# Optimization experiments

Hardware: AMD Instinct MI355X
Metric: run time of the kernel (lower is better)

## Reference

```python
import jax, jax.numpy as jnp
import numpy as np

NUM_HEADS = 16


def rotate_half(x):
    x1 = x[..., ::2]
    x2 = x[..., 1::2]
    return jnp.concatenate((-x2, x1), axis=-1)


def rope_sin_cos(seq_len, head_dim, dtype):
    inv_freq = 1.0 / (10000.0 ** (jnp.arange(0, head_dim, 2, dtype=jnp.float32) / head_dim))
    t = jnp.arange(seq_len, dtype=jnp.float32)
    freqs = jnp.einsum('i,j->ij', t, inv_freq)          # [S, D/2]
    emb = jnp.concatenate((freqs, freqs), axis=-1)      # [S, D]
    return jnp.sin(emb).astype(dtype), jnp.cos(emb).astype(dtype)


def setup_inputs() -> dict:
    key = jax.random.key(0)
    B, S, E = 2, 2048, 2048
    ks = jax.random.split(key, 5)
    scale = 1.0 / np.sqrt(E)
    return {
        'x': jax.random.normal(ks[0], (B, S, E), dtype=jnp.float32),
        'mask': jnp.ones((B, S), dtype=jnp.int32),
        'Wq': jax.random.normal(ks[1], (E, E), dtype=jnp.float32) * scale,
        'bq': jnp.zeros((E,), dtype=jnp.float32),
        'Wk': jax.random.normal(ks[2], (E, E), dtype=jnp.float32) * scale,
        'bk': jnp.zeros((E,), dtype=jnp.float32),
        'Wv': jax.random.normal(ks[3], (E, E), dtype=jnp.float32) * scale,
        'bv': jnp.zeros((E,), dtype=jnp.float32),
        'Wo': jax.random.normal(ks[4], (E, E), dtype=jnp.float32) * scale,
        'bo': jnp.zeros((E,), dtype=jnp.float32),
    }


def reference(x, mask, Wq, bq, Wk, bk, Wv, bv, Wo, bo):
    B, S, E = x.shape
    H = NUM_HEADS
    D = E // H
    q = (x @ Wq + bq).reshape(B, S, H, D).transpose(0, 2, 1, 3)  # [B,H,S,D]
    k = (x @ Wk + bk).reshape(B, S, H, D).transpose(0, 2, 1, 3)
    v = (x @ Wv + bv).reshape(B, S, H, D).transpose(0, 2, 1, 3)

    sin, cos = rope_sin_cos(S, D, q.dtype)  # [S,D]
    sin = sin[None, None]                    # [1,1,S,D]
    cos = cos[None, None]
    q = q * cos + rotate_half(q) * sin
    k = k * cos + rotate_half(k) * sin

    scores = jnp.einsum('bhqd,bhkd->bhqk', q, k) / jnp.sqrt(jnp.asarray(D, q.dtype))
    scores = jnp.where(mask[:, None, None, :] == 0, -jnp.inf, scores)
    probs = jax.nn.softmax(scores, axis=-1)
    attn = jnp.einsum('bhqk,bhkd->bhqd', probs, v)       # [B,H,S,D]
    attn = attn.transpose(0, 2, 1, 3).reshape(B, S, E)
    return attn @ Wo + bo
```

## Files before the change

kernel.cpp:

```cpp
#include <hip/hip_runtime.h>
#include <hip/hip_bf16.h>
#include <cmath>

typedef unsigned short u16;
typedef unsigned int   u32;

using v4f    = __attribute__((ext_vector_type(4)))  float;
using f32x16 = __attribute__((ext_vector_type(16))) float;
using s8v    = __attribute__((ext_vector_type(8)))  short;
using u32x2  = __attribute__((ext_vector_type(2)))  unsigned int;

union Frag { uint4 u; s8v s; };

__device__ __forceinline__ u16 f2bf(float f){
  u32 u = __float_as_uint(f);
  u32 r = u + 0x7fffu + ((u >> 16) & 1u);
  return (u16)(r >> 16);
}
__device__ __forceinline__ float bf2f(u16 h){ return __uint_as_float(((u32)h) << 16); }
__device__ __forceinline__ u32 pkbf(float a, float b){
  return (u32)f2bf(a) | ((u32)f2bf(b) << 16);
}

__device__ __forceinline__ void async16(const void* g, void* l){
  __builtin_amdgcn_global_load_lds((__attribute__((address_space(1))) void*)g,
                                   (__attribute__((address_space(3))) void*)l, 16, 0, 0);
}

__global__ __launch_bounds__(256) void cast_x_kernel(const float* __restrict__ x, u16* __restrict__ xb){
  size_t i = ((size_t)blockIdx.x * 256 + threadIdx.x) * 4;
  float4 v = *(const float4*)(x + i);
  uint2 o;
  o.x = (u32)f2bf(v.x) | ((u32)f2bf(v.y) << 16);
  o.y = (u32)f2bf(v.z) | ((u32)f2bf(v.w) << 16);
  *(uint2*)(xb + i) = o;
}

__global__ __launch_bounds__(256) void cast_transpose_kernel(
    const float* __restrict__ W0, const float* __restrict__ W1,
    const float* __restrict__ W2, const float* __restrict__ W3,
    u16* __restrict__ T0, u16* __restrict__ T1, u16* __restrict__ T2, u16* __restrict__ T3){
  __shared__ float tile[64][65];
  const float* W = (blockIdx.z==0)?W0:(blockIdx.z==1)?W1:(blockIdx.z==2)?W2:W3;
  u16*         T = (blockIdx.z==0)?T0:(blockIdx.z==1)?T1:(blockIdx.z==2)?T2:T3;
  const int k0 = blockIdx.y*64, n0 = blockIdx.x*64;
  const int t  = threadIdx.x;
  const int rr = t >> 4, c4 = (t & 15) * 4;
  #pragma unroll
  for (int i=0;i<4;i++){
    int k = rr + i*16;
    float4 v = *(const float4*)(W + (size_t)(k0+k)*2048 + n0 + c4);
    tile[k][c4+0]=v.x; tile[k][c4+1]=v.y; tile[k][c4+2]=v.z; tile[k][c4+3]=v.w;
  }
  __syncthreads();
  #pragma unroll
  for (int i=0;i<4;i++){
    int n = rr + i*16;
    uint2 o;
    o.x = (u32)f2bf(tile[c4+0][n]) | ((u32)f2bf(tile[c4+1][n])<<16);
    o.y = (u32)f2bf(tile[c4+2][n]) | ((u32)f2bf(tile[c4+3][n])<<16);
    *(uint2*)(T + (size_t)(n0+n)*2048 + k0 + c4) = o;
  }
}

template<int MODE>
__global__ __launch_bounds__(256) void gemm_kernel(const u16* __restrict__ A,
                                                   const u16* __restrict__ BT,
                                                   const float* __restrict__ bias,
                                                   void* __restrict__ Cout){
  constexpr int K = 2048;
  __shared__ u16 Asl[128*64];
  __shared__ u16 Bsl[128*64];
  const int tid  = threadIdx.x;
  const int w    = tid >> 6;
  const int lane = tid & 63;
  const int r    = lane & 15, q = lane >> 4;
  const int m0   = blockIdx.y * 128;
  const int n0   = blockIdx.x * 128;
  const int wm   = (w >> 1) * 64, wn = (w & 1) * 64;

  v4f acc[4][4];
  #pragma unroll
  for (int i=0;i<4;i++)
    #pragma unroll
    for (int j=0;j<4;j++) acc[i][j] = (v4f)0.f;

  const int srow = w*32 + (lane>>3);
  const int sblk = (lane&7) ^ ((lane>>3)&7);
  const u16* Ag = A  + (size_t)(m0+srow)*K + sblk*8;
  const u16* Bg = BT + (size_t)(n0+srow)*K + sblk*8;
  u16* Als = Asl + (w*32)*64;
  u16* Bls = Bsl + (w*32)*64;

  for (int kk = 0; kk < K; kk += 64) {
    #pragma unroll
    for (int i=0;i<4;i++){
      async16(Ag + (size_t)i*8*K + kk, Als + i*512);
      async16(Bg + (size_t)i*8*K + kk, Bls + i*512);
    }
    __syncthreads();
    #pragma unroll
    for (int ks=0; ks<2; ++ks) {
      s8v af[4], bfr[4];
      #pragma unroll
      for (int i=0;i<4;i++){
        int rho = wm + i*16 + r;
        int p = (ks*4 + q) ^ (r&7);
        Frag t; t.u = *(const uint4*)(Asl + rho*64 + p*8); af[i] = t.s;
      }
      #pragma unroll
      for (int j=0;j<4;j++){
        int rho = wn + j*16 + r;
        int p = (ks*4 + q) ^ (r&7);
        Frag t; t.u = *(const uint4*)(Bsl + rho*64 + p*8); bfr[j] = t.s;
      }
      #pragma unroll
      for (int i=0;i<4;i++)
        #pragma unroll
        for (int j=0;j<4;j++)
          acc[i][j] = __builtin_amdgcn_mfma_f32_16x16x32_bf16(af[i], bfr[j], acc[i][j], 0, 0, 0);
    }
    __syncthreads();
  }

  float bv[4];
  #pragma unroll
  for (int j=0;j<4;j++) bv[j] = bias[n0 + wn + j*16 + r];

  #pragma unroll
  for (int i=0;i<4;i++){
    #pragma unroll
    for (int j=0;j<4;j++){
      const int gn = n0 + wn + j*16 + r;
      #pragma unroll
      for (int rr2=0; rr2<4; ++rr2){
        const int gm = m0 + wm + i*16 + q*4 + rr2;
        float val = acc[i][j][rr2] + bv[j];
        if (MODE == 0) ((u16*)Cout)[(size_t)gm*2048 + gn] = f2bf(val);
        else           ((float*)Cout)[(size_t)gm*2048 + gn] = val;
      }
    }
  }
}

__global__ __launch_bounds__(256) void rope_kernel(u16* __restrict__ Q, u16* __restrict__ Kb){
  const int wrow = blockIdx.x*4 + (threadIdx.x >> 6);
  const int lane = threadIdx.x & 63;
  u16* P = (blockIdx.y == 0) ? Q : Kb;
  const int s = (wrow >> 4) & 2047;
  const size_t base = (size_t)wrow * 128;
  float invf = exp2f(-(float)lane * 0.20762050593045952f);
  float angle = (float)s * invf;
  float sn, cs;
  sincosf(angle, &sn, &cs);
  float x_j   = bf2f(P[base + lane]);
  float x_j64 = bf2f(P[base + 64 + lane]);
  float x_2j  = bf2f(P[base + 2*lane]);
  float x_2j1 = bf2f(P[base + 2*lane + 1]);
  float o0 = x_j  * cs - x_2j1 * sn;
  float o1 = x_j64 * cs + x_2j  * sn;
  P[base + lane]      = f2bf(o0);
  P[base + 64 + lane] = f2bf(o1);
}

__global__ __launch_bounds__(256) void transpose_v_kernel(const u16* __restrict__ V, u16* __restrict__ VT){
  __shared__ u16 t[64*72];
  const int s0 = blockIdx.x*64;
  const int d0 = blockIdx.y*64;
  const int bh = blockIdx.z;
  const int b = bh >> 4, h = bh & 15;
  const size_t obase = ((size_t)bh*128 + d0)*2048 + s0;
  const int tid = threadIdx.x;
  #pragma unroll
  for (int i=0;i<2;i++){
    int c = tid + i*256;
    int sl = c >> 3, dc = (c & 7) * 8;
    *(uint4*)(t + sl*72 + dc) =
      *(const uint4*)(V + ((size_t)(b*2048 + s0 + sl))*2048 + h*128 + d0 + dc);
  }
  __syncthreads();
  #pragma unroll
  for (int i=0;i<2;i++){
    int c = tid + i*256;
    int dl = c >> 3, sc4 = (c & 7) * 8;
    u16 tmp[8];
    #pragma unroll
    for (int j=0;j<8;j++) tmp[j] = t[(sc4+j)*72 + dl];
    *(uint4*)(VT + obase + (size_t)dl*2048 + sc4) = *(const uint4*)tmp;
  }
}

__global__ __launch_bounds__(256,2) void attn_kernel(const u16* __restrict__ Q,
                                                     const u16* __restrict__ K,
                                                     const u16* __restrict__ VT,
                                                     const int* __restrict__ mask,
                                                     u16* __restrict__ Out){
  constexpr int S = 2048;
  constexpr float SL2 = 0.08838834764831845f * 1.4426950408889634f;
  __shared__ u16 smem[16384];
  u16* Ks = smem;
  u16* Vs = smem + 8192;

  const int tid = threadIdx.x, w = tid >> 6, lane = tid & 63;
  const int qc = lane & 31;
  const int h  = lane >> 5;
  const int l7 = lane & 7;
  const int hh = blockIdx.y, b = blockIdx.z;
  const int q0 = blockIdx.x * 128;
  const size_t rowb = (size_t)b * 2048;
  const size_t bhD  = ((size_t)(b*16 + hh)) * 128;

  s8v qf[8];
  {
    const u16* qp = Q + (rowb + q0 + w*32 + qc)*2048 + hh*128 + h*8;
    #pragma unroll
    for (int t=0;t<8;t++){ Frag f; f.u = *(const uint4*)(qp + t*16); qf[t] = f.s; }
  }

  f32x16 accO[4];
  #pragma unroll
  for (int d=0; d<4; d++) accO[d] = (f32x16)0.f;
  float lsum = 0.f;

  const int sr4 = lane >> 4, sp16 = lane & 15;
  const int vr8 = lane >> 3, vp8 = lane & 7;

  for (int it=0; it<32; ++it){
    const int key0 = it*64;
    #pragma unroll
    for (int i=0;i<4;i++){
      int R = w*16 + i*4;
      int ob = sp16 ^ ((R&7) + sr4);
      async16(K + (rowb + key0 + R + sr4)*2048 + hh*128 + ob*8, Ks + R*128);
    }
    #pragma unroll
    for (int i=0;i<4;i++){
      int R = w*32 + i*8;
      int ob = vp8 ^ vr8;
      async16(VT + (bhD + R + vr8)*2048 + key0 + ob*8, Vs + R*64);
    }
    unsigned long long bm = __ballot(mask[b*S + key0 + lane] != 0);
    __syncthreads();

    #pragma unroll
    for (int nb=0; nb<2; ++nb){
      f32x16 sc = (f32x16)0.f;
      #pragma unroll
      for (int t=0;t<8;t++){
        Frag kf; kf.u = *(const uint4*)(Ks + (nb*32 + qc)*128 + (((2*t + h) ^ l7)*8));
        sc = __builtin_amdgcn_mfma_f32_32x32x16_bf16(kf.s, qf[t], sc, 0, 0, 0);
      }
      float p[16];
      #pragma unroll
      for (int m=0; m<16; ++m) p[m] = exp2f(sc[m] * SL2);
      if (bm != ~0ull){
        #pragma unroll
        for (int m=0; m<16; ++m){
          int bit = nb*32 + (m&3) + 8*(m>>2) + 4*h;
          if (!((bm >> bit) & 1ull)) p[m] = 0.f;
        }
      }
      #pragma unroll
      for (int m=0; m<16; ++m) lsum += p[m];

      #pragma unroll
      for (int g=0; g<2; ++g){
        u32 a0 = pkbf(p[8*g+0], p[8*g+1]);
        u32 a1 = pkbf(p[8*g+2], p[8*g+3]);
        u32 a2 = pkbf(p[8*g+4], p[8*g+5]);
        u32 a3 = pkbf(p[8*g+6], p[8*g+7]);
        u32x2 r0 = __builtin_amdgcn_permlane32_swap(a0, a2, false, false);
        u32x2 r1 = __builtin_amdgcn_permlane32_swap(a1, a3, false, false);
        Frag pf; pf.u = make_uint4(r0[0], r1[0], r0[1], r1[1]);
        const int T = nb*2 + g;
        #pragma unroll
        for (int d=0; d<4; ++d){
          Frag vf; vf.u = *(const uint4*)(Vs + (d*32 + qc)*64 + (((2*T + h) ^ l7)*8));
          accO[d] = __builtin_amdgcn_mfma_f32_32x32x16_bf16(vf.s, pf.s, accO[d], 0, 0, 0);
        }
      }
    }
    __syncthreads();
  }

  float sall = lsum + __shfl_xor(lsum, 32, 64);
  float invv = (sall > 0.f) ? 1.f/sall : 0.f;
  u16* orow = Out + (rowb + q0 + w*32 + qc)*2048 + hh*128;
  #pragma unroll
  for (int d=0; d<4; ++d){
    #pragma unroll
    for (int g2=0; g2<4; ++g2){
      union { u16 q4[4]; uint2 u; } o;
      #pragma unroll
      for (int j=0;j<4;j++) o.q4[j] = f2bf(accO[d][g2*4+j] * invv);
      *(uint2*)(orow + d*32 + g2*8 + 4*h) = o.u;
    }
  }
}

extern "C" void kernel_launch(void* const* d_in, const int* in_sizes, int n_in,
                              void* d_out, int out_size, void* d_ws, size_t ws_size,
                              hipStream_t stream) {
  (void)in_sizes; (void)n_in; (void)out_size; (void)ws_size;
  const float* x    = (const float*)d_in[0];
  const int*   mask = (const int*)d_in[1];
  const float* Wq   = (const float*)d_in[2];
  const float* bq   = (const float*)d_in[3];
  const float* Wk   = (const float*)d_in[4];
  const float* bk   = (const float*)d_in[5];
  const float* Wv   = (const float*)d_in[6];
  const float* bv   = (const float*)d_in[7];
  const float* Wo   = (const float*)d_in[8];
  const float* bo   = (const float*)d_in[9];

  u16* xbf = (u16*)d_ws;
  u16* WqT = xbf + 8388608;
  u16* WkT = WqT + 4194304;
  u16* WvT = WkT + 4194304;
  u16* WoT = WvT + 4194304;
  u16* Qb  = WoT + 4194304;
  u16* Kb  = Qb + 8388608;
  u16* Vb  = Kb + 8388608;
  u16* Ab  = Vb + 8388608;
  u16* VTb = Ab + 8388608;

  cast_x_kernel<<<8192, 256, 0, stream>>>(x, xbf);
  cast_transpose_kernel<<<dim3(32,32,4), 256, 0, stream>>>(Wq, Wk, Wv, Wo, WqT, WkT, WvT, WoT);
  gemm_kernel<0><<<dim3(16,32), 256, 0, stream>>>(xbf, WqT, bq, Qb);
  gemm_kernel<0><<<dim3(16,32), 256, 0, stream>>>(xbf, WkT, bk, Kb);
  gemm_kernel<0><<<dim3(16,32), 256, 0, stream>>>(xbf, WvT, bv, Vb);
  rope_kernel<<<dim3(16384,2), 256, 0, stream>>>(Qb, Kb);
  transpose_v_kernel<<<dim3(32,2,32), 256, 0, stream>>>(Vb, VTb);
  attn_kernel<<<dim3(16,16,2), 256, 0, stream>>>(Qb, Kb, VTb, mask, Ab);
  gemm_kernel<1><<<dim3(16,32), 256, 0, stream>>>(Ab, WoT, bo, (float*)d_out);
}
```

Baseline: 428.9 us.

## Double-buffer K/V tiles in attention, use hardware bf16 pack and MFMA priority

The attention kernel now keeps two LDS buffers for K/V tiles and issues the async load for the next 64-key tile before computing on the current one, so global-to-LDS latency overlaps the MFMA work. The mask load for the next tile is issued early in the same way. Software bf16 rounding is replaced by the v_cvt_pk_bf16_f32 instruction, and s_setprio raises wave priority around the MFMA loops. Doubling LDS to 64KB per block may cut occupancy below the two blocks per CU the launch bounds target.

```diff
diff --git a/kernel.cpp b/kernel.cpp
--- a/kernel.cpp
+++ b/kernel.cpp
@@ -18,8 +18,11 @@
   return (u16)(r >> 16);
 }
 __device__ __forceinline__ float bf2f(u16 h){ return __uint_as_float(((u32)h) << 16); }
-__device__ __forceinline__ u32 pkbf(float a, float b){
-  return (u32)f2bf(a) | ((u32)f2bf(b) << 16);
+
+__device__ __forceinline__ u32 cvtpk(float a, float b){
+  u32 r;
+  asm("v_cvt_pk_bf16_f32 %0, %1, %2" : "=v"(r) : "v"(a), "v"(b));
+  return r;
 }
 
 __device__ __forceinline__ void async16(const void* g, void* l){
@@ -197,9 +200,7 @@
                                                      u16* __restrict__ Out){
   constexpr int S = 2048;
   constexpr float SL2 = 0.08838834764831845f * 1.4426950408889634f;
-  __shared__ u16 smem[16384];
-  u16* Ks = smem;
-  u16* Vs = smem + 8192;
+  __shared__ u16 smem[32768];
 
   const int tid = threadIdx.x, w = tid >> 6, lane = tid & 63;
   const int qc = lane & 31;
@@ -225,31 +226,47 @@
   const int sr4 = lane >> 4, sp16 = lane & 15;
   const int vr8 = lane >> 3, vp8 = lane & 7;
 
-  for (int it=0; it<32; ++it){
-    const int key0 = it*64;
+  auto stage = [&](u16* base, int key0){
+    u16* Kd = base;
+    u16* Vd = base + 8192;
     #pragma unroll
     for (int i=0;i<4;i++){
       int R = w*16 + i*4;
       int ob = sp16 ^ ((R&7) + sr4);
-      async16(K + (rowb + key0 + R + sr4)*2048 + hh*128 + ob*8, Ks + R*128);
+      async16(K + (rowb + key0 + R + sr4)*2048 + hh*128 + ob*8, Kd + R*128);
     }
     #pragma unroll
     for (int i=0;i<4;i++){
       int R = w*32 + i*8;
       int ob = vp8 ^ vr8;
-      async16(VT + (bhD + R + vr8)*2048 + key0 + ob*8, Vs + R*64);
-    }
-    unsigned long long bm = __ballot(mask[b*S + key0 + lane] != 0);
-    __syncthreads();
+      async16(VT + (bhD + R + vr8)*2048 + key0 + ob*8, Vd + R*64);
+    }
+  };
+
+  stage(smem, 0);
+  int mv = mask[b*S + lane];
+  __syncthreads();
+  unsigned long long bm = __ballot(mv != 0);
+  int cur = 0;
+
+  for (int it=0; it<32; ++it){
+    if (it < 31){
+      stage(smem + (cur^1)*16384, (it+1)*64);
+      mv = mask[b*S + (it+1)*64 + lane];
+    }
+    const u16* Ks = smem + cur*16384;
+    const u16* Vs = Ks + 8192;
 
     #pragma unroll
     for (int nb=0; nb<2; ++nb){
       f32x16 sc = (f32x16)0.f;
+      __builtin_amdgcn_s_setprio(1);
       #pragma unroll
       for (int t=0;t<8;t++){
         Frag kf; kf.u = *(const uint4*)(Ks + (nb*32 + qc)*128 + (((2*t + h) ^ l7)*8));
         sc = __builtin_amdgcn_mfma_f32_32x32x16_bf16(kf.s, qf[t], sc, 0, 0, 0);
       }
+      __builtin_amdgcn_s_setprio(0);
       float p[16];
       #pragma unroll
       for (int m=0; m<16; ++m) p[m] = exp2f(sc[m] * SL2);
@@ -265,22 +282,26 @@
 
       #pragma unroll
       for (int g=0; g<2; ++g){
-        u32 a0 = pkbf(p[8*g+0], p[8*g+1]);
-        u32 a1 = pkbf(p[8*g+2], p[8*g+3]);
-        u32 a2 = pkbf(p[8*g+4], p[8*g+5]);
-        u32 a3 = pkbf(p[8*g+6], p[8*g+7]);
+        u32 a0 = cvtpk(p[8*g+0], p[8*g+1]);
+        u32 a1 = cvtpk(p[8*g+2], p[8*g+3]);
+        u32 a2 = cvtpk(p[8*g+4], p[8*g+5]);
+        u32 a3 = cvtpk(p[8*g+6], p[8*g+7]);
         u32x2 r0 = __builtin_amdgcn_permlane32_swap(a0, a2, false, false);
         u32x2 r1 = __builtin_amdgcn_permlane32_swap(a1, a3, false, false);
         Frag pf; pf.u = make_uint4(r0[0], r1[0], r0[1], r1[1]);
         const int T = nb*2 + g;
+        __builtin_amdgcn_s_setprio(1);
         #pragma unroll
         for (int d=0; d<4; ++d){
           Frag vf; vf.u = *(const uint4*)(Vs + (d*32 + qc)*64 + (((2*T + h) ^ l7)*8));
           accO[d] = __builtin_amdgcn_mfma_f32_32x32x16_bf16(vf.s, pf.s, accO[d], 0, 0, 0);
         }
+        __builtin_amdgcn_s_setprio(0);
       }
     }
     __syncthreads();
+    bm = __ballot(mv != 0);
+    cur ^= 1;
   }
 
   float sall = lsum + __shfl_xor(lsum, 32, 64);
@@ -290,10 +311,10 @@
   for (int d=0; d<4; ++d){
     #pragma unroll
     for (int g2=0; g2<4; ++g2){
-      union { u16 q4[4]; uint2 u; } o;
-      #pragma unroll
-      for (int j=0;j<4;j++) o.q4[j] = f2bf(accO[d][g2*4+j] * invv);
-      *(uint2*)(orow + d*32 + g2*8 + 4*h) = o.u;
+      uint2 o;
+      o.x = cvtpk(accO[d][g2*4+0] * invv, accO[d][g2*4+1] * invv);
+      o.y = cvtpk(accO[d][g2*4+2] * invv, accO[d][g2*4+3] * invv);
+      *(uint2*)(orow + d*32 + g2*8 + 4*h) = o;
     }
   }
 }
```

New measurement: 436.1 us. About the same (+1.7%).
